# Kernel optimization log

Measured on AMD Instinct MI355X. Metric: run time of the kernel, lower is better.

The kernel has to match this reference:

```python
import jax, jax.numpy as jnp
import numpy as np

B, S, D = 4, 2048, 2048
NH, NKV = 16, 4
HD = D // NH            # 128
DKV = NKV * HD          # 512
REP = NH // NKV         # 4
SCALE = HD ** -0.5
EPS = 1e-9


def setup_inputs() -> dict:
    key = jax.random.key(0)
    ks = jax.random.split(key, 9)
    s = 0.02
    return {
        "q": jax.random.normal(ks[0], (B, S, D), jnp.float32),
        "k": jax.random.normal(ks[1], (B, S, D), jnp.float32),
        "v": jax.random.normal(ks[2], (B, S, D), jnp.float32),
        "Wq": jax.random.normal(ks[3], (D, D), jnp.float32) * s,
        "bq": jnp.zeros((D,), jnp.float32),
        "Wk": jax.random.normal(ks[4], (D, DKV), jnp.float32) * s,
        "bk": jnp.zeros((DKV,), jnp.float32),
        "Wv": jax.random.normal(ks[5], (D, DKV), jnp.float32) * s,
        "bv": jnp.zeros((DKV,), jnp.float32),
    }


def reference(q, k, v, Wq, bq, Wk, bk, Wv, bv):
    # Dense projections (nn.Dense = x @ W + b)
    qh = q @ Wq + bq                      # (B, S, D)
    kh = k @ Wk + bk                      # (B, S, DKV)
    vh = v @ Wv + bv                      # (B, S, DKV)
    # Faithful to source: repeat along axis=-2 (the SEQUENCE axis)
    kh = jnp.repeat(kh, REP, axis=-2)     # (B, S*REP, DKV)
    vh = jnp.repeat(vh, REP, axis=-2)     # (B, S*REP, DKV)
    # flash_attention math: reshape to (B, S, NH, HD) -> (B, NH, S, HD)
    qh = qh.reshape(B, S, NH, HD).transpose(0, 2, 1, 3)
    kh = kh.reshape(B, S, NH, HD).transpose(0, 2, 1, 3)
    vh = vh.reshape(B, S, NH, HD).transpose(0, 2, 1, 3)
    attn = jnp.einsum("bhqd,bhkd->bhqk", qh, kh) * SCALE
    m = jnp.max(attn, axis=-1, keepdims=True)
    e = jnp.exp(attn - m)
    p = e / (jnp.sum(e, axis=-1, keepdims=True) + EPS)
    out = jnp.einsum("bhqk,bhkd->bhqd", p, vh)   # (B, NH, S, HD)
    return out.transpose(0, 2, 1, 3).reshape(B, S, D)
```

## Files before the change

kernel.cpp:

```cpp
#include <hip/hip_runtime.h>

#define B_    4
#define S_    2048
#define D_    2048
#define NH_   16
#define NKV_  4
#define HD_   128
#define DKV_  512
#define QSCALE_ ((float)(0.08838834764831845 * 1.4426950408889634))

typedef __attribute__((ext_vector_type(8))) short          bf16x8;
typedef __attribute__((ext_vector_type(8))) unsigned short us8;
typedef __attribute__((ext_vector_type(4))) unsigned short us4;
typedef __attribute__((ext_vector_type(4))) float          f32x4;

__device__ __forceinline__ unsigned short f2bf(float f) {
    union { float f; unsigned int u; } v; v.f = f;
    unsigned int u = v.u;
    u += 0x7fffu + ((u >> 16) & 1u);
    return (unsigned short)(u >> 16);
}

__device__ __forceinline__ unsigned int cvt_pk_bf16(float lo, float hi) {
    unsigned int r;
    asm volatile("v_cvt_pk_bf16_f32 %0, %1, %2" : "=v"(r) : "v"(lo), "v"(hi));
    return r;
}

__device__ __forceinline__ float vmax3(float a, float b, float c) {
    float r;
    asm("v_max3_f32 %0, %1, %2, %3" : "=v"(r) : "v"(a), "v"(b), "v"(c));
    return r;
}

#define GLOAD16(gp, lp) __builtin_amdgcn_global_load_lds(                      \
    (const __attribute__((address_space(1))) unsigned int*)(gp),              \
    (__attribute__((address_space(3))) unsigned int*)(lp), 16, 0, 0)

__device__ __forceinline__ void tr_body(
    const float* __restrict__ W, unsigned short* __restrict__ WT,
    int K, int N, int kb, int nb, float (*tile)[33])
{
    const int k0 = kb * 32, n0 = nb * 32;
    const int tx = threadIdx.x & 31, ty = threadIdx.x >> 5;
#pragma unroll
    for (int i = 0; i < 32; i += 8)
        tile[ty + i][tx] = W[(size_t)(k0 + ty + i) * N + n0 + tx];
    __syncthreads();
#pragma unroll
    for (int i = 0; i < 32; i += 8)
        WT[(size_t)(n0 + ty + i) * K + k0 + tx] = f2bf(tile[tx][ty + i]);
}

__global__ __launch_bounds__(256) void transpose_all(
    const float* __restrict__ Wq, const float* __restrict__ Wk,
    const float* __restrict__ Wv, unsigned short* __restrict__ WqT,
    unsigned short* __restrict__ WkT, unsigned short* __restrict__ WvT)
{
    __shared__ float tile[32][33];
    const int y = blockIdx.y;
    if (y < 64)       tr_body(Wq, WqT, D_, D_,   blockIdx.x, y,      tile);
    else if (y < 80)  tr_body(Wk, WkT, D_, DKV_, blockIdx.x, y - 64, tile);
    else              tr_body(Wv, WvT, D_, DKV_, blockIdx.x, y - 80, tile);
}

__device__ __forceinline__ void gemm_body(
    const float* __restrict__ A, const unsigned short* __restrict__ BT,
    const float* __restrict__ bias, unsigned short* __restrict__ C,
    int N, int nb, float scale, int vmode,
    unsigned short* As , unsigned short* Bs )
{
    const int K = D_;
    const int m0 = blockIdx.x * 128, n0 = nb * 128;
    const int t = threadIdx.x;
    const int w = t >> 6, l = t & 63, lr = l & 15, lg = l >> 4;
    const int wr = (w >> 1) * 64, wc = (w & 1) * 64;
    const int srA = t >> 1, scA = (t & 1) * 16;
    const int srB = t >> 2, scB = (t & 3) * 8;

    const float* aptr = A + (size_t)(m0 + srA) * K + scA;
    const unsigned short* bS = BT + (size_t)(n0 + srB) * K + scB;

    float4 pa0, pa1, pa2, pa3;
    auto prefA = [&](int k0) {
        const float4* ap = (const float4*)(aptr + k0);
        pa0 = ap[0]; pa1 = ap[1]; pa2 = ap[2]; pa3 = ap[3];
    };

    f32x4 acc[4][4] = {};
    prefA(0);
    const int nk = K / 32;
    for (int kt = 0; kt < nk; ++kt) {
        __syncthreads();
        GLOAD16(bS + kt * 32,                  &Bs[t * 8]);
        GLOAD16(bS + (size_t)64 * K + kt * 32, &Bs[2048 + t * 8]);
        uint2 c0, c1;
        c0.x = cvt_pk_bf16(pa0.x, pa0.y); c0.y = cvt_pk_bf16(pa0.z, pa0.w);
        c1.x = cvt_pk_bf16(pa1.x, pa1.y); c1.y = cvt_pk_bf16(pa1.z, pa1.w);
        *(uint2*)&As[srA * 40 + scA]     = c0;
        *(uint2*)&As[srA * 40 + scA + 4] = c1;
        c0.x = cvt_pk_bf16(pa2.x, pa2.y); c0.y = cvt_pk_bf16(pa2.z, pa2.w);
        c1.x = cvt_pk_bf16(pa3.x, pa3.y); c1.y = cvt_pk_bf16(pa3.z, pa3.w);
        *(uint2*)&As[srA * 40 + scA + 8]  = c0;
        *(uint2*)&As[srA * 40 + scA + 12] = c1;
        __syncthreads();
        if (kt + 1 < nk) prefA((kt + 1) * 32);

        bf16x8 af[4], bfv[4];
#pragma unroll
        for (int i = 0; i < 4; ++i)
            af[i] = *(const bf16x8*)&As[(wr + i * 16 + lr) * 40 + lg * 8];
#pragma unroll
        for (int i = 0; i < 4; ++i)
            bfv[i] = *(const bf16x8*)&Bs[(wc + i * 16 + lr) * 32 + lg * 8];
#pragma unroll
        for (int i = 0; i < 4; ++i)
#pragma unroll
            for (int j = 0; j < 4; ++j)
                acc[i][j] = __builtin_amdgcn_mfma_f32_16x16x32_bf16(
                    af[i], bfv[j], acc[i][j], 0, 0, 0);
    }

#pragma unroll
    for (int j = 0; j < 4; ++j) {
        const int col = n0 + wc + j * 16 + lr;
        const float bv = bias[col];
#pragma unroll
        for (int i = 0; i < 4; ++i) {
            const int row0 = m0 + wr + i * 16 + lg * 4;
            if (vmode == 0) {
#pragma unroll
                for (int r = 0; r < 4; ++r)
                    C[(size_t)(row0 + r) * N + col] = f2bf((acc[i][j][r] + bv) * scale);
            } else {
                const int bb = row0 >> 11, s0 = row0 & (S_ - 1);
                us4 hv;
#pragma unroll
                for (int r = 0; r < 4; ++r) hv[r] = f2bf((acc[i][j][r] + bv) * scale);
                *(us4*)&C[((size_t)bb * N + col) * S_ + s0] = hv;
            }
        }
    }
}

__global__ __launch_bounds__(256) void gemm_all(
    const float* __restrict__ q, const float* __restrict__ k,
    const float* __restrict__ v,
    const unsigned short* __restrict__ WqT, const unsigned short* __restrict__ WkT,
    const unsigned short* __restrict__ WvT,
    const float* __restrict__ bq, const float* __restrict__ bk,
    const float* __restrict__ bv,
    unsigned short* __restrict__ qh, unsigned short* __restrict__ kh,
    unsigned short* __restrict__ vhT)
{
    __shared__ __align__(16) unsigned short As[128 * 40];
    __shared__ __align__(16) unsigned short Bs[128 * 32];
    const int y = blockIdx.y;
    if (y < 16)      gemm_body(q, WqT, bq, qh,  D_,   y,      QSCALE_, 0, As, Bs);
    else if (y < 20) gemm_body(k, WkT, bk, kh,  DKV_, y - 16, 1.0f,    0, As, Bs);
    else             gemm_body(v, WvT, bv, vhT, DKV_, y - 20, 1.0f,    1, As, Bs);
}

__global__ __launch_bounds__(256, 2) void attn_kernel(
    const unsigned short* __restrict__ qh, const unsigned short* __restrict__ kh,
    const unsigned short* __restrict__ vhT, float* __restrict__ out)
{
    __shared__ __align__(16) unsigned short Kd[2][64 * 128];
    __shared__ __align__(16) unsigned short Vd[2][128 * 64];
    __shared__ __align__(16) unsigned int   P2T[4][16 * 44];

    const int qb = blockIdx.x, h = blockIdx.y, b = blockIdx.z;
    const int g = h & (NKV_ - 1);
    const int t = threadIdx.x, w = t >> 6, l = t & 63, lr = l & 15, lg = l >> 4;
    const int q0 = qb * 128 + w * 32;

    bf16x8 qf[2][4];
#pragma unroll
    for (int rf = 0; rf < 2; ++rf) {
        const unsigned short* qrow =
            qh + ((size_t)(b * S_) + q0 + rf * 16 + lr) * D_ + h * HD_;
#pragma unroll
        for (int ko = 0; ko < 4; ++ko)
            qf[rf][ko] = *(const bf16x8*)(qrow + ko * 32 + lg * 8);
    }

    bf16x8 onesf;
#pragma unroll
    for (int j = 0; j < 8; ++j) onesf[j] = (short)0x3F80;

    f32x4 o[2][8] = {};
    f32x4 oe[2] = {};
    float mrow[2] = {-1e30f, -1e30f};

    const unsigned short* kb_ = kh + (size_t)b * S_ * DKV_ + g * HD_;
    const unsigned short* vb_ = vhT + ((size_t)b * DKV_ + g * HD_) * S_;

    const int kc = ((t & 15) * 8) ^ (((t >> 4) & 7) << 3);
    const int vc = ((t & 7) * 8) ^ (((t >> 3) & 7) << 3);

    auto stage = [&](int buf, int kt) {
        const unsigned short* ks = kb_ + (size_t)(kt * 64) * DKV_ + kc;
        const unsigned short* vs = vb_ + kt * 64 + vc;
#pragma unroll
        for (int i = 0; i < 4; ++i)
            GLOAD16(ks + (size_t)(i * 16 + (t >> 4)) * DKV_, &Kd[buf][i * 2048 + t * 8]);
#pragma unroll
        for (int i = 0; i < 4; ++i)
            GLOAD16(vs + (size_t)(i * 32 + (t >> 3)) * S_,   &Vd[buf][i * 2048 + t * 8]);
    };

    stage(0, 0);
    stage(1, 1);

    const int swz = (lr & 7) << 3;
    unsigned int* pw = &P2T[w][lr * 44];
    int cur = 0;
    const int NT = S_ / 64;
    for (int kt = 0; kt < NT; ++kt) {
        if (kt + 1 < NT) { asm volatile("s_waitcnt vmcnt(8)" ::: "memory"); }
        else             { asm volatile("s_waitcnt vmcnt(0)" ::: "memory"); }
        __builtin_amdgcn_s_barrier();
        __builtin_amdgcn_sched_barrier(0);

        f32x4 sa[2][4] = {};
        __builtin_amdgcn_s_setprio(1);
#pragma unroll
        for (int cf = 0; cf < 4; ++cf)
#pragma unroll
            for (int ko = 0; ko < 4; ++ko) {
                bf16x8 kf = *(const bf16x8*)
                    &Kd[cur][(cf * 16 + lr) * 128 + ((ko * 32 + lg * 8) ^ swz)];
                sa[0][cf] = __builtin_amdgcn_mfma_f32_16x16x32_bf16(kf, qf[0][ko], sa[0][cf], 0, 0, 0);
                sa[1][cf] = __builtin_amdgcn_mfma_f32_16x16x32_bf16(kf, qf[1][ko], sa[1][cf], 0, 0, 0);
            }
        __builtin_amdgcn_s_setprio(0);

        bf16x8 pa[2][2];
#pragma unroll
        for (int rf = 0; rf < 2; ++rf) {
            const float m0v = vmax3(sa[rf][0][0], sa[rf][0][1], sa[rf][0][2]);
            const float m1v = vmax3(sa[rf][0][3], sa[rf][1][0], sa[rf][1][1]);
            const float m2v = vmax3(sa[rf][1][2], sa[rf][1][3], sa[rf][2][0]);
            const float m3v = vmax3(sa[rf][2][1], sa[rf][2][2], sa[rf][2][3]);
            const float m4v = vmax3(sa[rf][3][0], sa[rf][3][1], sa[rf][3][2]);
            const float mxl = fmaxf(vmax3(m0v, m1v, m2v),
                                    vmax3(m3v, m4v, sa[rf][3][3]));
            float m = mrow[rf];
            if (!__all(mxl <= m + 8.f)) {
                float mx = fmaxf(mxl, m);
                mx = fmaxf(mx, __shfl_xor(mx, 16));
                mx = fmaxf(mx, __shfl_xor(mx, 32));
                const float al = exp2f(m - mx);
                mrow[rf] = m = mx;
#pragma unroll
                for (int r = 0; r < 4; ++r) {
                    const float a = __shfl(al, lg * 4 + r);
                    oe[rf][r] *= a;
#pragma unroll
                    for (int df = 0; df < 8; ++df) o[rf][df][r] *= a;
                }
            }
            float p[4][4];
#pragma unroll
            for (int cf = 0; cf < 4; ++cf)
#pragma unroll
                for (int r = 0; r < 4; ++r)
                    p[cf][r] = exp2f(sa[rf][cf][r] - m);
#pragma unroll
            for (int cf = 0; cf < 4; ++cf) {
                uint2 pk;
                pk.x = cvt_pk_bf16(p[cf][0], p[cf][1]);
                pk.y = cvt_pk_bf16(p[cf][2], p[cf][3]);
                *(uint2*)&pw[cf * 8 + lg * 2] = pk;
            }
            pa[rf][0] = *(const bf16x8*)&pw[lg * 4];
            pa[rf][1] = *(const bf16x8*)&pw[16 + lg * 4];
        }

        __builtin_amdgcn_s_setprio(1);
#pragma unroll
        for (int ks = 0; ks < 2; ++ks)
#pragma unroll
            for (int df = 0; df < 8; ++df) {
                bf16x8 vf = *(const bf16x8*)
                    &Vd[cur][(df * 16 + lr) * 64 + ((ks * 32 + lg * 8) ^ swz)];
                o[0][df] = __builtin_amdgcn_mfma_f32_16x16x32_bf16(pa[0][ks], vf, o[0][df], 0, 0, 0);
                o[1][df] = __builtin_amdgcn_mfma_f32_16x16x32_bf16(pa[1][ks], vf, o[1][df], 0, 0, 0);
            }
        oe[0] = __builtin_amdgcn_mfma_f32_16x16x32_bf16(pa[0][0], onesf, oe[0], 0, 0, 0);
        oe[0] = __builtin_amdgcn_mfma_f32_16x16x32_bf16(pa[0][1], onesf, oe[0], 0, 0, 0);
        oe[1] = __builtin_amdgcn_mfma_f32_16x16x32_bf16(pa[1][0], onesf, oe[1], 0, 0, 0);
        oe[1] = __builtin_amdgcn_mfma_f32_16x16x32_bf16(pa[1][1], onesf, oe[1], 0, 0, 0);
        __builtin_amdgcn_s_setprio(0);

        __builtin_amdgcn_sched_barrier(0);
        __builtin_amdgcn_s_barrier();
        __builtin_amdgcn_sched_barrier(0);
        if (kt + 2 < NT) stage(cur, kt + 2);
        cur ^= 1;
    }

#pragma unroll
    for (int rf = 0; rf < 2; ++rf) {
        float* ob = out + ((size_t)(b * S_) + q0 + rf * 16 + lg * 4) * D_ + h * HD_;
#pragma unroll
        for (int r = 0; r < 4; ++r) {
            const float inv = 1.f / (oe[rf][r] + 1e-9f);
#pragma unroll
            for (int df = 0; df < 8; ++df)
                ob[(size_t)r * D_ + df * 16 + lr] = o[rf][df][r] * inv;
        }
    }
}

extern "C" void kernel_launch(void* const* d_in, const int* in_sizes, int n_in,
                              void* d_out, int out_size, void* d_ws, size_t ws_size,
                              hipStream_t stream)
{
    const float* q  = (const float*)d_in[0];
    const float* k  = (const float*)d_in[1];
    const float* v  = (const float*)d_in[2];
    const float* Wq = (const float*)d_in[3];
    const float* bq = (const float*)d_in[4];
    const float* Wk = (const float*)d_in[5];
    const float* bk = (const float*)d_in[6];
    const float* Wv = (const float*)d_in[7];
    const float* bv = (const float*)d_in[8];
    float* out = (float*)d_out;

    char* ws = (char*)d_ws;
    unsigned short* qh  = (unsigned short*)ws; ws += (size_t)B_ * S_ * D_ * 2;
    unsigned short* kh  = (unsigned short*)ws; ws += (size_t)B_ * S_ * DKV_ * 2;
    unsigned short* vhT = (unsigned short*)ws; ws += (size_t)B_ * DKV_ * S_ * 2;
    unsigned short* WqT = (unsigned short*)ws; ws += (size_t)D_ * D_ * 2;
    unsigned short* WkT = (unsigned short*)ws; ws += (size_t)DKV_ * D_ * 2;
    unsigned short* WvT = (unsigned short*)ws; ws += (size_t)DKV_ * D_ * 2;

    transpose_all<<<dim3(64, 96), 256, 0, stream>>>(Wq, Wk, Wv, WqT, WkT, WvT);

    const int M = B_ * S_;
    gemm_all<<<dim3(M / 128, 24), 256, 0, stream>>>(
        q, k, v, WqT, WkT, WvT, bq, bk, bv, qh, kh, vhT);

    attn_kernel<<<dim3(S_ / 128, NH_, B_), 256, 0, stream>>>(qh, kh, vhT, out);
}
```

Baseline: 395.0 us.

## Double-buffer GEMM A tiles via direct LDS loads; shuffle P fragments in attention

The projection GEMM now stages fp32 A tiles straight into swizzled LDS with global_load_lds into a double buffer. The bf16 conversion moves to fragment-read time, removing the register prefetch and one barrier per k-step. In attention, the per-wave LDS round-trip that rearranged P into MFMA A-operand layout is replaced by cross-lane shuffles. V fragment reads are permuted to match the new k ordering. The cost is larger GEMM LDS use (fp32 A, two buffers) and repeated conversion work per wave.

```diff
diff --git a/kernel.cpp b/kernel.cpp
--- a/kernel.cpp
+++ b/kernel.cpp
@@ -33,6 +33,13 @@
     return r;
 }
 
+__device__ __forceinline__ bf16x8 pack4(unsigned int a, unsigned int b,
+                                        unsigned int c, unsigned int d) {
+    union { unsigned int u[4]; bf16x8 v; } x;
+    x.u[0] = a; x.u[1] = b; x.u[2] = c; x.u[3] = d;
+    return x.v;
+}
+
 #define GLOAD16(gp, lp) __builtin_amdgcn_global_load_lds(                      \
     (const __attribute__((address_space(1))) unsigned int*)(gp),              \
     (__attribute__((address_space(3))) unsigned int*)(lp), 16, 0, 0)
@@ -68,57 +75,62 @@
     const float* __restrict__ A, const unsigned short* __restrict__ BT,
     const float* __restrict__ bias, unsigned short* __restrict__ C,
     int N, int nb, float scale, int vmode,
-    unsigned short* As , unsigned short* Bs )
+    float* Asf , unsigned short* Bs )
 {
     const int K = D_;
     const int m0 = blockIdx.x * 128, n0 = nb * 128;
     const int t = threadIdx.x;
     const int w = t >> 6, l = t & 63, lr = l & 15, lg = l >> 4;
     const int wr = (w >> 1) * 64, wc = (w & 1) * 64;
-    const int srA = t >> 1, scA = (t & 1) * 16;
     const int srB = t >> 2, scB = (t & 3) * 8;
 
-    const float* aptr = A + (size_t)(m0 + srA) * K + scA;
     const unsigned short* bS = BT + (size_t)(n0 + srB) * K + scB;
 
-    float4 pa0, pa1, pa2, pa3;
-    auto prefA = [&](int k0) {
-        const float4* ap = (const float4*)(aptr + k0);
-        pa0 = ap[0]; pa1 = ap[1]; pa2 = ap[2]; pa3 = ap[3];
+    auto stage = [&](int buf, int kt) {
+#pragma unroll
+        for (int i = 0; i < 4; ++i) {
+            const int ch = i * 256 + t;
+            const int row = ch >> 3, pc = ch & 7;
+            const int lc = pc ^ (row & 7);
+            GLOAD16(A + (size_t)(m0 + row) * K + kt * 32 + lc * 4,
+                    &Asf[buf * 4096 + ch * 4]);
+        }
+        GLOAD16(bS + kt * 32,                  &Bs[buf * 4096 + t * 8]);
+        GLOAD16(bS + (size_t)64 * K + kt * 32, &Bs[buf * 4096 + 2048 + t * 8]);
     };
 
     f32x4 acc[4][4] = {};
-    prefA(0);
+    stage(0, 0);
+    __syncthreads();
+
     const int nk = K / 32;
+    int cur = 0;
     for (int kt = 0; kt < nk; ++kt) {
-        __syncthreads();
-        GLOAD16(bS + kt * 32,                  &Bs[t * 8]);
-        GLOAD16(bS + (size_t)64 * K + kt * 32, &Bs[2048 + t * 8]);
-        uint2 c0, c1;
-        c0.x = cvt_pk_bf16(pa0.x, pa0.y); c0.y = cvt_pk_bf16(pa0.z, pa0.w);
-        c1.x = cvt_pk_bf16(pa1.x, pa1.y); c1.y = cvt_pk_bf16(pa1.z, pa1.w);
-        *(uint2*)&As[srA * 40 + scA]     = c0;
-        *(uint2*)&As[srA * 40 + scA + 4] = c1;
-        c0.x = cvt_pk_bf16(pa2.x, pa2.y); c0.y = cvt_pk_bf16(pa2.z, pa2.w);
-        c1.x = cvt_pk_bf16(pa3.x, pa3.y); c1.y = cvt_pk_bf16(pa3.z, pa3.w);
-        *(uint2*)&As[srA * 40 + scA + 8]  = c0;
-        *(uint2*)&As[srA * 40 + scA + 12] = c1;
-        __syncthreads();
-        if (kt + 1 < nk) prefA((kt + 1) * 32);
+        if (kt + 1 < nk) stage(cur ^ 1, kt + 1);
 
         bf16x8 af[4], bfv[4];
 #pragma unroll
+        for (int i = 0; i < 4; ++i) {
+            const int row = wr + i * 16 + lr;
+            const int r7 = row & 7;
+            const float* rp = &Asf[cur * 4096 + row * 32];
+            f32x4 a0 = *(const f32x4*)&rp[((2 * lg) ^ r7) * 4];
+            f32x4 a1 = *(const f32x4*)&rp[((2 * lg + 1) ^ r7) * 4];
+            af[i] = pack4(cvt_pk_bf16(a0[0], a0[1]), cvt_pk_bf16(a0[2], a0[3]),
+                          cvt_pk_bf16(a1[0], a1[1]), cvt_pk_bf16(a1[2], a1[3]));
+        }
+#pragma unroll
         for (int i = 0; i < 4; ++i)
-            af[i] = *(const bf16x8*)&As[(wr + i * 16 + lr) * 40 + lg * 8];
-#pragma unroll
-        for (int i = 0; i < 4; ++i)
-            bfv[i] = *(const bf16x8*)&Bs[(wc + i * 16 + lr) * 32 + lg * 8];
+            bfv[i] = *(const bf16x8*)&Bs[cur * 4096 + (wc + i * 16 + lr) * 32 + lg * 8];
 #pragma unroll
         for (int i = 0; i < 4; ++i)
 #pragma unroll
             for (int j = 0; j < 4; ++j)
                 acc[i][j] = __builtin_amdgcn_mfma_f32_16x16x32_bf16(
                     af[i], bfv[j], acc[i][j], 0, 0, 0);
+
+        __syncthreads();
+        cur ^= 1;
     }
 
 #pragma unroll
@@ -153,12 +165,12 @@
     unsigned short* __restrict__ qh, unsigned short* __restrict__ kh,
     unsigned short* __restrict__ vhT)
 {
-    __shared__ __align__(16) unsigned short As[128 * 40];
-    __shared__ __align__(16) unsigned short Bs[128 * 32];
+    __shared__ __align__(16) float          Asf[2 * 128 * 32];
+    __shared__ __align__(16) unsigned short Bs[2 * 128 * 32];
     const int y = blockIdx.y;
-    if (y < 16)      gemm_body(q, WqT, bq, qh,  D_,   y,      QSCALE_, 0, As, Bs);
-    else if (y < 20) gemm_body(k, WkT, bk, kh,  DKV_, y - 16, 1.0f,    0, As, Bs);
-    else             gemm_body(v, WvT, bv, vhT, DKV_, y - 20, 1.0f,    1, As, Bs);
+    if (y < 16)      gemm_body(q, WqT, bq, qh,  D_,   y,      QSCALE_, 0, Asf, Bs);
+    else if (y < 20) gemm_body(k, WkT, bk, kh,  DKV_, y - 16, 1.0f,    0, Asf, Bs);
+    else             gemm_body(v, WvT, bv, vhT, DKV_, y - 20, 1.0f,    1, Asf, Bs);
 }
 
 __global__ __launch_bounds__(256, 2) void attn_kernel(
@@ -167,12 +179,13 @@
 {
     __shared__ __align__(16) unsigned short Kd[2][64 * 128];
     __shared__ __align__(16) unsigned short Vd[2][128 * 64];
-    __shared__ __align__(16) unsigned int   P2T[4][16 * 44];
 
     const int qb = blockIdx.x, h = blockIdx.y, b = blockIdx.z;
     const int g = h & (NKV_ - 1);
     const int t = threadIdx.x, w = t >> 6, l = t & 63, lr = l & 15, lg = l >> 4;
     const int q0 = qb * 128 + w * 32;
+    const bool godd = (lg & 1) != 0;
+    const int sU8 = ((((lg & 1) ^ 1) << 1) + (lg >> 1)) * 8;
 
     bf16x8 qf[2][4];
 #pragma unroll
@@ -213,7 +226,6 @@
     stage(1, 1);
 
     const int swz = (lr & 7) << 3;
-    unsigned int* pw = &P2T[w][lr * 44];
     int cur = 0;
     const int NT = S_ / 64;
     for (int kt = 0; kt < NT; ++kt) {
@@ -266,27 +278,38 @@
 #pragma unroll
                 for (int r = 0; r < 4; ++r)
                     p[cf][r] = exp2f(sa[rf][cf][r] - m);
+            unsigned int xp[4][2];
 #pragma unroll
             for (int cf = 0; cf < 4; ++cf) {
-                uint2 pk;
-                pk.x = cvt_pk_bf16(p[cf][0], p[cf][1]);
-                pk.y = cvt_pk_bf16(p[cf][2], p[cf][3]);
-                *(uint2*)&pw[cf * 8 + lg * 2] = pk;
-            }
-            pa[rf][0] = *(const bf16x8*)&pw[lg * 4];
-            pa[rf][1] = *(const bf16x8*)&pw[16 + lg * 4];
+                xp[cf][0] = cvt_pk_bf16(p[cf][0], p[cf][1]);
+                xp[cf][1] = cvt_pk_bf16(p[cf][2], p[cf][3]);
+            }
+#pragma unroll
+            for (int pi = 0; pi < 2; ++pi) {
+                const int c0 = pi * 2, c1 = c0 + 1;
+                const int t0 = __shfl_xor((int)xp[c0][0], 16);
+                const int u0 = __shfl_xor((int)xp[c1][0], 16);
+                const int t1 = __shfl_xor((int)xp[c0][1], 16);
+                const int u1 = __shfl_xor((int)xp[c1][1], 16);
+                const unsigned int e0 = godd ? (unsigned int)t0 : xp[c1][0];
+                const unsigned int e1 = godd ? (unsigned int)t1 : xp[c1][1];
+                const unsigned int o0 = godd ? xp[c0][0] : (unsigned int)u0;
+                const unsigned int o1 = godd ? xp[c0][1] : (unsigned int)u1;
+                pa[rf][pi] = pack4(e0, e1, o0, o1);
+            }
         }
 
         __builtin_amdgcn_s_setprio(1);
 #pragma unroll
-        for (int ks = 0; ks < 2; ++ks)
-#pragma unroll
-            for (int df = 0; df < 8; ++df) {
-                bf16x8 vf = *(const bf16x8*)
-                    &Vd[cur][(df * 16 + lr) * 64 + ((ks * 32 + lg * 8) ^ swz)];
-                o[0][df] = __builtin_amdgcn_mfma_f32_16x16x32_bf16(pa[0][ks], vf, o[0][df], 0, 0, 0);
-                o[1][df] = __builtin_amdgcn_mfma_f32_16x16x32_bf16(pa[1][ks], vf, o[1][df], 0, 0, 0);
-            }
+        for (int df = 0; df < 8; ++df) {
+            const int rbase = (df * 16 + lr) * 64;
+            bf16x8 vfU = *(const bf16x8*)&Vd[cur][rbase + (sU8 ^ swz)];
+            bf16x8 vfW = *(const bf16x8*)&Vd[cur][rbase + ((sU8 + 32) ^ swz)];
+            o[0][df] = __builtin_amdgcn_mfma_f32_16x16x32_bf16(pa[0][0], vfU, o[0][df], 0, 0, 0);
+            o[1][df] = __builtin_amdgcn_mfma_f32_16x16x32_bf16(pa[1][0], vfU, o[1][df], 0, 0, 0);
+            o[0][df] = __builtin_amdgcn_mfma_f32_16x16x32_bf16(pa[0][1], vfW, o[0][df], 0, 0, 0);
+            o[1][df] = __builtin_amdgcn_mfma_f32_16x16x32_bf16(pa[1][1], vfW, o[1][df], 0, 0, 0);
+        }
         oe[0] = __builtin_amdgcn_mfma_f32_16x16x32_bf16(pa[0][0], onesf, oe[0], 0, 0, 0);
         oe[0] = __builtin_amdgcn_mfma_f32_16x16x32_bf16(pa[0][1], onesf, oe[0], 0, 0, 0);
         oe[1] = __builtin_amdgcn_mfma_f32_16x16x32_bf16(pa[1][0], onesf, oe[1], 0, 0, 0);
```

Result: slower. 436.1 us (+10.4%).
